# Kernel tuning notes

Measured on AMD Instinct MI355X. Metric: run time of the kernel, lower is better.

The kernel has to match this reference:

```python
import jax, jax.numpy as jnp
import numpy as np


def setup_inputs() -> dict:
    key = jax.random.key(0)
    k0, k1, k2, k3 = jax.random.split(key, 4)
    B, N, D, C, F = 8192, 784, 64, 10, 2  # batch, input_dim, bond_dim, num_classes, feature_dim
    x = jax.random.uniform(k0, (B, N), dtype=jnp.float32)  # pixel values in [0,1]
    core0 = jax.random.normal(k1, (F, 1, D), dtype=jnp.float32) * 0.1
    base = jnp.broadcast_to(jnp.eye(D, dtype=jnp.float32), (N - 2, F, D, D))
    cores_mid = base + jax.random.normal(k2, (N - 2, F, D, D), dtype=jnp.float32) * 0.01
    core_last = jax.random.normal(k3, (F, D, C), dtype=jnp.float32) * 0.1
    return {"x": x, "core0": core0, "cores_mid": cores_mid, "core_last": core_last}


def reference(x, core0, cores_mid, core_last):
    EPS = 1e-8
    factor = jnp.float32(np.pi / 2.0)
    # FeatureMap: [B, N] -> [B, N, 2] with (cos, sin)
    feats = jnp.stack([jnp.cos(factor * x), jnp.sin(factor * x)], axis=-1)
    # First site: M = v0 @ A0.squeeze(1)  -> [B, D]
    M = jnp.einsum('bf,fd->bd', feats[:, 0, :], core0[:, 0, :])
    # Sequential left->right contraction over middle sites with per-step L2 normalization
    v_mid = jnp.moveaxis(feats[:, 1:-1, :], 1, 0)  # [N-2, B, 2]

    def step(M, inp):
        v, A = inp  # v: [B, 2], A: [2, D, D]
        Mn = jnp.einsum('bi,bf,fij->bj', M, v, A)
        Mn = Mn / (jnp.linalg.norm(Mn, axis=1, keepdims=True) + EPS)
        return Mn, None

    M, _ = jax.lax.scan(step, M, (v_mid, cores_mid))
    # Last site: logits[b,c] = sum_i M[b,i] * (v_N[b,f] A_N[f,i,c])
    logits = jnp.einsum('bi,bf,fic->bc', M, feats[:, -1, :], core_last)
    return logits
```

## Files before the change

kernel.cpp:

```cpp
#include <hip/hip_runtime.h>

typedef __attribute__((ext_vector_type(8))) short s16x8;
typedef __attribute__((ext_vector_type(4))) float f32x4;
typedef __attribute__((ext_vector_type(4))) int i32x4;

#define NMID 782
#define PI_2 1.5707963267948966f
#define EG_STEP_BYTES 16384
#define EG_ELEMS ((size_t)NMID * 8192)
#define SLAB_B 2304

__device__ __forceinline__ int cvt_pk_bf16(float a, float b) {
  int r;
  asm("v_cvt_pk_bf16_f32 %0, %1, %2" : "=v"(r) : "v"(a), "v"(b));
  return r;
}

__device__ __forceinline__ f32x4 mfma_bf16(i32x4 a, i32x4 b, f32x4 c) {
  return __builtin_amdgcn_mfma_f32_16x16x32_bf16(
      __builtin_bit_cast(s16x8, a), __builtin_bit_cast(s16x8, b), c, 0, 0, 0);
}

__device__ __forceinline__ unsigned short bf16_rne(float v) {
  unsigned u = __float_as_uint(v);
  return (unsigned short)((u + 0x7FFFu + ((u >> 16) & 1)) >> 16);
}

__global__ __launch_bounds__(256) void prep_eg(const float* __restrict__ cm,
                                               unsigned short* __restrict__ eg) {
  const int n = blockIdx.x;
  const float* src = cm + (size_t)n * 8192;
  unsigned short* dst = eg + (size_t)n * 8192;
#pragma unroll
  for (int it = 0; it < 4; ++it) {
    int row = it * 256 + threadIdx.x;
    int q = row >> 6, l = row & 63;
    int t = q >> 2, cc = q & 3;
    int f = cc >> 1, c2 = cc & 1, h = l >> 4;
    int j = 16 * t + (l & 15);
    unsigned short v8[8];
#pragma unroll
    for (int e = 0; e < 8; ++e) {
      int i = 32 * c2 + 16 * (e >> 2) + 4 * h + (e & 3);
      float val = src[(f * 64 + i) * 64 + j] - (i == j ? 1.0f : 0.0f);
      v8[e] = bf16_rne(val);
    }
    *(uint4*)(dst + (size_t)row * 8) = *(const uint4*)v8;
  }
}

#define STEP4(nc, CUR, NXT, CC, SS)                                         \
  {                                                                         \
    int np = (nc) + 3;                                                      \
    if (np >= NMID) np = NMID - 1;                                          \
    const char* pnxt = base + (size_t)np * EG_STEP_BYTES;                   \
    _Pragma("unroll") for (int q = 0; q < 4; ++q)                           \
        NXT[q] = *(const i32x4*)(pnxt + q * 1024);                          \
    float cps = (CC) + (SS);                                                \
    f32x4 z = {0.f, 0.f, 0.f, 0.f};                                         \
    f32x4 accA = mfma_bf16(CUR[0], B0, z);                                  \
    accA = mfma_bf16(CUR[1], B1, accA);                                     \
    f32x4 accB = mfma_bf16(CUR[2], B0, z);                                  \
    accB = mfma_bf16(CUR[3], B1, accB);                                     \
    f32x4 mn;                                                               \
    _Pragma("unroll") for (int r = 0; r < 4; ++r)                           \
        mn[r] = cps * own4[r] + (CC)*accA[r] + (SS)*accB[r];                \
    own4 = mn;                                                              \
    int2 wq;                                                                \
    wq.x = cvt_pk_bf16(mn[0], mn[1]);                                       \
    wq.y = cvt_pk_bf16(mn[2], mn[3]);                                       \
    *(int2*)(xlds + (((nc) + 1) & 1) * SLAB_B + bl * 144 + h * 32 +         \
             wv * 8) = wq;                                                  \
    asm volatile("s_waitcnt lgkmcnt(0)" ::: "memory");                      \
    __builtin_amdgcn_s_barrier();                                           \
    __builtin_amdgcn_sched_barrier(0);                                      \
    {                                                                       \
      const char* rb =                                                      \
          xlds + (((nc) + 1) & 1) * SLAB_B + bl * 144 + h * 32;             \
      B0 = *(const i32x4*)(rb);                                             \
      B1 = *(const i32x4*)(rb + 16);                                        \
    }                                                                       \
  }

__global__ __launch_bounds__(256) void mps_main(
    const float* __restrict__ x, const float* __restrict__ core0,
    const float* __restrict__ core_last, const unsigned short* __restrict__ eg,
    float* __restrict__ out) {
  __shared__ alignas(16) char xlds[2 * SLAB_B];
  const int lane = threadIdx.x & 63;
  const int wv = threadIdx.x >> 6;
  const int bl = lane & 15;
  const int h = lane >> 4;
  const int b = blockIdx.x * 16 + bl;
  const float* xr = x + (size_t)b * 784;
  const char* base = (const char*)eg + (size_t)wv * 4096 + (size_t)lane * 16;

  f32x4 own4;
  i32x4 B0, B1;
  {
    float xv = xr[0];
    float s, c;
    __sincosf(PI_2 * xv, &s, &c);
    float fm[16];
#pragma unroll
    for (int t = 0; t < 4; ++t)
#pragma unroll
      for (int r = 0; r < 4; ++r) {
        int j = 16 * t + 4 * h + r;
        fm[t * 4 + r] = c * core0[j] + s * core0[64 + j];
      }
#pragma unroll
    for (int r = 0; r < 4; ++r) own4[r] = fm[wv * 4 + r];
#pragma unroll
    for (int p = 0; p < 4; ++p) {
      B0[p] = cvt_pk_bf16(fm[2 * p], fm[2 * p + 1]);
      B1[p] = cvt_pk_bf16(fm[8 + 2 * p], fm[8 + 2 * p + 1]);
    }
  }

  i32x4 frA[4], frB[4], frC[4], frD[4];
#pragma unroll
  for (int q = 0; q < 4; ++q)
    frA[q] = *(const i32x4*)(base + 0 * EG_STEP_BYTES + q * 1024);
#pragma unroll
  for (int q = 0; q < 4; ++q)
    frB[q] = *(const i32x4*)(base + 1 * EG_STEP_BYTES + q * 1024);
#pragma unroll
  for (int q = 0; q < 4; ++q)
    frC[q] = *(const i32x4*)(base + 2 * EG_STEP_BYTES + q * 1024);

  float xq[12], xqn[12];
  *(f32x4*)&xq[0] = *(const f32x4*)(xr + 0);
  *(f32x4*)&xq[4] = *(const f32x4*)(xr + 4);
  *(f32x4*)&xq[8] = *(const f32x4*)(xr + 8);

  for (int g = 0; g < 97; ++g) {
    if (g < 96) {
      const float* xp = xr + 8 * (g + 1);
      *(f32x4*)&xqn[0] = *(const f32x4*)(xp + 0);
      *(f32x4*)&xqn[4] = *(const f32x4*)(xp + 4);
      *(f32x4*)&xqn[8] = *(const f32x4*)(xp + 8);
    } else {
      *(f32x4*)&xqn[0] = *(const f32x4*)(xr + 776);
      *(f32x4*)&xqn[4] = *(const f32x4*)(xr + 780);
    }

    float cg[8], sg[8];
#pragma unroll
    for (int k = 0; k < 8; ++k) __sincosf(PI_2 * xq[1 + k], &sg[k], &cg[k]);

    if ((g & 7) == 0) {
      float ss = 0.f;
#pragma unroll
      for (int p = 0; p < 4; ++p) {
        unsigned u0 = (unsigned)B0[p], u1 = (unsigned)B1[p];
        float a0 = __uint_as_float(u0 << 16);
        float a1 = __uint_as_float(u0 & 0xFFFF0000u);
        float b0f = __uint_as_float(u1 << 16);
        float b1f = __uint_as_float(u1 & 0xFFFF0000u);
        ss += a0 * a0 + a1 * a1 + b0f * b0f + b1f * b1f;
      }
      ss += __shfl_xor(ss, 16);
      ss += __shfl_xor(ss, 32);
      float inv = rsqrtf(ss);
      cg[0] *= inv;
      sg[0] *= inv;
    }

    int n0 = 8 * g;
    STEP4(n0 + 0, frA, frD, cg[0], sg[0]);
    STEP4(n0 + 1, frB, frA, cg[1], sg[1]);
    STEP4(n0 + 2, frC, frB, cg[2], sg[2]);
    STEP4(n0 + 3, frD, frC, cg[3], sg[3]);
    STEP4(n0 + 4, frA, frD, cg[4], sg[4]);
    STEP4(n0 + 5, frB, frA, cg[5], sg[5]);
    STEP4(n0 + 6, frC, frB, cg[6], sg[6]);
    STEP4(n0 + 7, frD, frC, cg[7], sg[7]);

#pragma unroll
    for (int i = 0; i < 12; ++i) xq[i] = xqn[i];
  }

  {
    float cg[6], sg[6];
#pragma unroll
    for (int k = 0; k < 6; ++k) __sincosf(PI_2 * xq[1 + k], &sg[k], &cg[k]);
    STEP4(776, frA, frD, cg[0], sg[0]);
    STEP4(777, frB, frA, cg[1], sg[1]);
    STEP4(778, frC, frB, cg[2], sg[2]);
    STEP4(779, frD, frC, cg[3], sg[3]);
    STEP4(780, frA, frD, cg[4], sg[4]);
    STEP4(781, frB, frA, cg[5], sg[5]);
  }

  asm volatile("s_waitcnt lgkmcnt(0)" ::: "memory");
  __builtin_amdgcn_s_barrier();
  *(f32x4*)(xlds + wv * 1152 + lane * 16) = own4;
  asm volatile("s_waitcnt lgkmcnt(0)" ::: "memory");
  __builtin_amdgcn_s_barrier();
  __builtin_amdgcn_sched_barrier(0);
  float fm[16];
#pragma unroll
  for (int t = 0; t < 4; ++t) {
    f32x4 v = *(const f32x4*)(xlds + t * 1152 + lane * 16);
#pragma unroll
    for (int r = 0; r < 4; ++r) fm[t * 4 + r] = v[r];
  }

  float ss = 0.f;
#pragma unroll
  for (int i = 0; i < 16; ++i) ss += fm[i] * fm[i];
  ss += __shfl_xor(ss, 16);
  ss += __shfl_xor(ss, 32);
  float inv = 1.0f / (sqrtf(ss) + 1e-8f);
#pragma unroll
  for (int i = 0; i < 16; ++i) fm[i] *= inv;

  float xv = xq[7];
  float s, c;
  __sincosf(PI_2 * xv, &s, &c);
  float part[10];
#pragma unroll
  for (int cc = 0; cc < 10; ++cc) part[cc] = 0.f;
#pragma unroll
  for (int t = 0; t < 4; ++t)
#pragma unroll
    for (int r = 0; r < 4; ++r) {
      int i = 16 * t + 4 * h + r;
      float mv = fm[t * 4 + r];
#pragma unroll
      for (int cc = 0; cc < 10; ++cc)
        part[cc] += mv * (c * core_last[i * 10 + cc] + s * core_last[640 + i * 10 + cc]);
    }
#pragma unroll
  for (int cc = 0; cc < 10; ++cc) {
    part[cc] += __shfl_xor(part[cc], 16);
    part[cc] += __shfl_xor(part[cc], 32);
  }
  if (wv == 0 && h == 0) {
#pragma unroll
    for (int cc = 0; cc < 10; ++cc) out[b * 10 + cc] = part[cc];
  }
}

__global__ __launch_bounds__(64) void mps_slow(const float* __restrict__ x,
                                               const float* __restrict__ core0,
                                               const float* __restrict__ cm,
                                               const float* __restrict__ cl,
                                               float* __restrict__ out) {
  int b = blockIdx.x * 64 + threadIdx.x;
  float m[64], mn[64];
  float s, c;
  __sincosf(PI_2 * x[(size_t)b * 784], &s, &c);
  for (int d = 0; d < 64; ++d) m[d] = c * core0[d] + s * core0[64 + d];
  for (int n = 0; n < NMID; ++n) {
    __sincosf(PI_2 * x[(size_t)b * 784 + n + 1], &s, &c);
    const float* A0 = cm + (size_t)n * 8192;
    const float* A1 = A0 + 4096;
    for (int j = 0; j < 64; ++j) mn[j] = 0.f;
    for (int i = 0; i < 64; ++i) {
      float w0 = c * m[i], w1 = s * m[i];
      for (int j = 0; j < 64; ++j) mn[j] += w0 * A0[i * 64 + j] + w1 * A1[i * 64 + j];
    }
    float ssn = 0.f;
    for (int j = 0; j < 64; ++j) ssn += mn[j] * mn[j];
    float inv = 1.f / (sqrtf(ssn) + 1e-8f);
    for (int j = 0; j < 64; ++j) m[j] = mn[j] * inv;
  }
  __sincosf(PI_2 * x[(size_t)b * 784 + 783], &s, &c);
  for (int cc = 0; cc < 10; ++cc) {
    float acc = 0.f;
    for (int i = 0; i < 64; ++i)
      acc += m[i] * (c * cl[i * 10 + cc] + s * cl[640 + i * 10 + cc]);
    out[b * 10 + cc] = acc;
  }
}

extern "C" void kernel_launch(void* const* d_in, const int* in_sizes, int n_in,
                              void* d_out, int out_size, void* d_ws, size_t ws_size,
                              hipStream_t stream) {
  const float* x = (const float*)d_in[0];
  const float* core0 = (const float*)d_in[1];
  const float* cm = (const float*)d_in[2];
  const float* cl = (const float*)d_in[3];
  float* out = (float*)d_out;
  size_t need = EG_ELEMS * sizeof(unsigned short);
  if (ws_size >= need) {
    unsigned short* eg = (unsigned short*)d_ws;
    prep_eg<<<NMID, 256, 0, stream>>>(cm, eg);
    mps_main<<<512, 256, 0, stream>>>(x, core0, cl, eg, out);
  } else {
    mps_slow<<<8192 / 64, 64, 0, stream>>>(x, core0, cm, cl, out);
  }
}
```

Measured before the change: 267.9 us.

## Process two batch groups per block to reuse core fragments across MFMAs

```diff
diff --git a/kernel.cpp b/kernel.cpp
--- a/kernel.cpp
+++ b/kernel.cpp
@@ -9,6 +9,7 @@
 #define EG_STEP_BYTES 16384
 #define EG_ELEMS ((size_t)NMID * 8192)
 #define SLAB_B 2304
+#define DBUF_B 4608
 
 __device__ __forceinline__ int cvt_pk_bf16(float a, float b) {
   int r;
@@ -49,58 +50,77 @@
   }
 }
 
-#define STEP4(nc, CUR, NXT, CC, SS)                                         \
+#define STEP2G(nc, CUR, NXT, C0, S0, C1, S1)                                \
   {                                                                         \
     int np = (nc) + 3;                                                      \
     if (np >= NMID) np = NMID - 1;                                          \
     const char* pnxt = base + (size_t)np * EG_STEP_BYTES;                   \
     _Pragma("unroll") for (int q = 0; q < 4; ++q)                           \
         NXT[q] = *(const i32x4*)(pnxt + q * 1024);                          \
-    float cps = (CC) + (SS);                                                \
     f32x4 z = {0.f, 0.f, 0.f, 0.f};                                         \
-    f32x4 accA = mfma_bf16(CUR[0], B0, z);                                  \
-    accA = mfma_bf16(CUR[1], B1, accA);                                     \
-    f32x4 accB = mfma_bf16(CUR[2], B0, z);                                  \
-    accB = mfma_bf16(CUR[3], B1, accB);                                     \
-    f32x4 mn;                                                               \
+    __builtin_amdgcn_s_setprio(1);                                          \
+    f32x4 aA0 = mfma_bf16(CUR[0], B0g0, z);                                 \
+    aA0 = mfma_bf16(CUR[1], B1g0, aA0);                                     \
+    f32x4 aB0 = mfma_bf16(CUR[2], B0g0, z);                                 \
+    aB0 = mfma_bf16(CUR[3], B1g0, aB0);                                     \
+    f32x4 aA1 = mfma_bf16(CUR[0], B0g1, z);                                 \
+    aA1 = mfma_bf16(CUR[1], B1g1, aA1);                                     \
+    f32x4 aB1 = mfma_bf16(CUR[2], B0g1, z);                                 \
+    aB1 = mfma_bf16(CUR[3], B1g1, aB1);                                     \
+    __builtin_amdgcn_s_setprio(0);                                          \
+    char* wb = xlds + (((nc) + 1) & 1) * DBUF_B + bl * 144 + h * 32 +       \
+               wv * 8;                                                      \
+    float cps0 = (C0) + (S0);                                               \
+    f32x4 mn0;                                                              \
     _Pragma("unroll") for (int r = 0; r < 4; ++r)                           \
-        mn[r] = cps * own4[r] + (CC)*accA[r] + (SS)*accB[r];                \
-    own4 = mn;                                                              \
-    int2 wq;                                                                \
-    wq.x = cvt_pk_bf16(mn[0], mn[1]);                                       \
-    wq.y = cvt_pk_bf16(mn[2], mn[3]);                                       \
-    *(int2*)(xlds + (((nc) + 1) & 1) * SLAB_B + bl * 144 + h * 32 +         \
-             wv * 8) = wq;                                                  \
+        mn0[r] = cps0 * own0[r] + (C0)*aA0[r] + (S0)*aB0[r];                \
+    own0 = mn0;                                                             \
+    int2 w0;                                                                \
+    w0.x = cvt_pk_bf16(mn0[0], mn0[1]);                                     \
+    w0.y = cvt_pk_bf16(mn0[2], mn0[3]);                                     \
+    *(int2*)(wb) = w0;                                                      \
+    float cps1 = (C1) + (S1);                                               \
+    f32x4 mn1;                                                              \
+    _Pragma("unroll") for (int r = 0; r < 4; ++r)                           \
+        mn1[r] = cps1 * own1[r] + (C1)*aA1[r] + (S1)*aB1[r];                \
+    own1 = mn1;                                                             \
+    int2 w1;                                                                \
+    w1.x = cvt_pk_bf16(mn1[0], mn1[1]);                                     \
+    w1.y = cvt_pk_bf16(mn1[2], mn1[3]);                                     \
+    *(int2*)(wb + SLAB_B) = w1;                                             \
     asm volatile("s_waitcnt lgkmcnt(0)" ::: "memory");                      \
     __builtin_amdgcn_s_barrier();                                           \
     __builtin_amdgcn_sched_barrier(0);                                      \
     {                                                                       \
       const char* rb =                                                      \
-          xlds + (((nc) + 1) & 1) * SLAB_B + bl * 144 + h * 32;             \
-      B0 = *(const i32x4*)(rb);                                             \
-      B1 = *(const i32x4*)(rb + 16);                                        \
+          xlds + (((nc) + 1) & 1) * DBUF_B + bl * 144 + h * 32;             \
+      B0g0 = *(const i32x4*)(rb);                                           \
+      B1g0 = *(const i32x4*)(rb + 16);                                      \
+      B0g1 = *(const i32x4*)(rb + SLAB_B);                                  \
+      B1g1 = *(const i32x4*)(rb + SLAB_B + 16);                             \
     }                                                                       \
   }
 
-__global__ __launch_bounds__(256) void mps_main(
+__global__ __launch_bounds__(256, 1) void mps_main(
     const float* __restrict__ x, const float* __restrict__ core0,
     const float* __restrict__ core_last, const unsigned short* __restrict__ eg,
     float* __restrict__ out) {
-  __shared__ alignas(16) char xlds[2 * SLAB_B];
+  __shared__ alignas(16) char xlds[2 * DBUF_B];
   const int lane = threadIdx.x & 63;
   const int wv = threadIdx.x >> 6;
   const int bl = lane & 15;
   const int h = lane >> 4;
-  const int b = blockIdx.x * 16 + bl;
-  const float* xr = x + (size_t)b * 784;
+  const int b0 = blockIdx.x * 32 + bl;
+  const int b1 = b0 + 16;
+  const float* xr0 = x + (size_t)b0 * 784;
+  const float* xr1 = x + (size_t)b1 * 784;
   const char* base = (const char*)eg + (size_t)wv * 4096 + (size_t)lane * 16;
 
-  f32x4 own4;
-  i32x4 B0, B1;
+  f32x4 own0, own1;
+  i32x4 B0g0, B1g0, B0g1, B1g1;
   {
-    float xv = xr[0];
     float s, c;
-    __sincosf(PI_2 * xv, &s, &c);
+    __sincosf(PI_2 * xr0[0], &s, &c);
     float fm[16];
 #pragma unroll
     for (int t = 0; t < 4; ++t)
@@ -110,11 +130,30 @@
         fm[t * 4 + r] = c * core0[j] + s * core0[64 + j];
       }
 #pragma unroll
-    for (int r = 0; r < 4; ++r) own4[r] = fm[wv * 4 + r];
+    for (int r = 0; r < 4; ++r) own0[r] = fm[wv * 4 + r];
 #pragma unroll
     for (int p = 0; p < 4; ++p) {
-      B0[p] = cvt_pk_bf16(fm[2 * p], fm[2 * p + 1]);
-      B1[p] = cvt_pk_bf16(fm[8 + 2 * p], fm[8 + 2 * p + 1]);
+      B0g0[p] = cvt_pk_bf16(fm[2 * p], fm[2 * p + 1]);
+      B1g0[p] = cvt_pk_bf16(fm[8 + 2 * p], fm[8 + 2 * p + 1]);
+    }
+  }
+  {
+    float s, c;
+    __sincosf(PI_2 * xr1[0], &s, &c);
+    float fm[16];
+#pragma unroll
+    for (int t = 0; t < 4; ++t)
+#pragma unroll
+      for (int r = 0; r < 4; ++r) {
+        int j = 16 * t + 4 * h + r;
+        fm[t * 4 + r] = c * core0[j] + s * core0[64 + j];
+      }
+#pragma unroll
+    for (int r = 0; r < 4; ++r) own1[r] = fm[wv * 4 + r];
+#pragma unroll
+    for (int p = 0; p < 4; ++p) {
+      B0g1[p] = cvt_pk_bf16(fm[2 * p], fm[2 * p + 1]);
+      B1g1[p] = cvt_pk_bf16(fm[8 + 2 * p], fm[8 + 2 * p + 1]);
     }
   }
 
@@ -129,117 +168,153 @@
   for (int q = 0; q < 4; ++q)
     frC[q] = *(const i32x4*)(base + 2 * EG_STEP_BYTES + q * 1024);
 
-  float xq[12], xqn[12];
-  *(f32x4*)&xq[0] = *(const f32x4*)(xr + 0);
-  *(f32x4*)&xq[4] = *(const f32x4*)(xr + 4);
-  *(f32x4*)&xq[8] = *(const f32x4*)(xr + 8);
-
-  for (int g = 0; g < 97; ++g) {
-    if (g < 96) {
-      const float* xp = xr + 8 * (g + 1);
-      *(f32x4*)&xqn[0] = *(const f32x4*)(xp + 0);
-      *(f32x4*)&xqn[4] = *(const f32x4*)(xp + 4);
-      *(f32x4*)&xqn[8] = *(const f32x4*)(xp + 8);
+  float xq0[16], xqn0[16], xq1[16], xqn1[16];
+  *(f32x4*)&xq0[0] = *(const f32x4*)(xr0 + 0);
+  *(f32x4*)&xq0[4] = *(const f32x4*)(xr0 + 4);
+  *(f32x4*)&xq0[8] = *(const f32x4*)(xr0 + 8);
+  *(f32x4*)&xq0[12] = *(const f32x4*)(xr0 + 12);
+  *(f32x4*)&xq1[0] = *(const f32x4*)(xr1 + 0);
+  *(f32x4*)&xq1[4] = *(const f32x4*)(xr1 + 4);
+  *(f32x4*)&xq1[8] = *(const f32x4*)(xr1 + 8);
+  *(f32x4*)&xq1[12] = *(const f32x4*)(xr1 + 12);
+
+  for (int g = 0; g < 65; ++g) {
+    if (g < 64) {
+      const float* xp0 = xr0 + 12 * (g + 1);
+      *(f32x4*)&xqn0[0] = *(const f32x4*)(xp0 + 0);
+      *(f32x4*)&xqn0[4] = *(const f32x4*)(xp0 + 4);
+      *(f32x4*)&xqn0[8] = *(const f32x4*)(xp0 + 8);
+      *(f32x4*)&xqn0[12] = *(const f32x4*)(xp0 + 12);
+      const float* xp1 = xr1 + 12 * (g + 1);
+      *(f32x4*)&xqn1[0] = *(const f32x4*)(xp1 + 0);
+      *(f32x4*)&xqn1[4] = *(const f32x4*)(xp1 + 4);
+      *(f32x4*)&xqn1[8] = *(const f32x4*)(xp1 + 8);
+      *(f32x4*)&xqn1[12] = *(const f32x4*)(xp1 + 12);
     } else {
-      *(f32x4*)&xqn[0] = *(const f32x4*)(xr + 776);
-      *(f32x4*)&xqn[4] = *(const f32x4*)(xr + 780);
-    }
-
-    float cg[8], sg[8];
-#pragma unroll
-    for (int k = 0; k < 8; ++k) __sincosf(PI_2 * xq[1 + k], &sg[k], &cg[k]);
-
-    if ((g & 7) == 0) {
-      float ss = 0.f;
+      *(f32x4*)&xqn0[0] = *(const f32x4*)(xr0 + 780);
+      *(f32x4*)&xqn1[0] = *(const f32x4*)(xr1 + 780);
+    }
+
+    float cg0[12], sg0[12], cg1[12], sg1[12];
+#pragma unroll
+    for (int k = 0; k < 12; ++k) {
+      __sincosf(PI_2 * xq0[1 + k], &sg0[k], &cg0[k]);
+      __sincosf(PI_2 * xq1[1 + k], &sg1[k], &cg1[k]);
+    }
+
+    if (g % 5 == 0) {
+      float ss0 = 0.f, ss1 = 0.f;
 #pragma unroll
       for (int p = 0; p < 4; ++p) {
-        unsigned u0 = (unsigned)B0[p], u1 = (unsigned)B1[p];
+        unsigned u0 = (unsigned)B0g0[p], u1 = (unsigned)B1g0[p];
         float a0 = __uint_as_float(u0 << 16);
         float a1 = __uint_as_float(u0 & 0xFFFF0000u);
-        float b0f = __uint_as_float(u1 << 16);
-        float b1f = __uint_as_float(u1 & 0xFFFF0000u);
-        ss += a0 * a0 + a1 * a1 + b0f * b0f + b1f * b1f;
+        float d0 = __uint_as_float(u1 << 16);
+        float d1 = __uint_as_float(u1 & 0xFFFF0000u);
+        ss0 += a0 * a0 + a1 * a1 + d0 * d0 + d1 * d1;
+        unsigned v0 = (unsigned)B0g1[p], v1 = (unsigned)B1g1[p];
+        float e0 = __uint_as_float(v0 << 16);
+        float e1 = __uint_as_float(v0 & 0xFFFF0000u);
+        float f0 = __uint_as_float(v1 << 16);
+        float f1 = __uint_as_float(v1 & 0xFFFF0000u);
+        ss1 += e0 * e0 + e1 * e1 + f0 * f0 + f1 * f1;
       }
-      ss += __shfl_xor(ss, 16);
-      ss += __shfl_xor(ss, 32);
-      float inv = rsqrtf(ss);
-      cg[0] *= inv;
-      sg[0] *= inv;
-    }
-
-    int n0 = 8 * g;
-    STEP4(n0 + 0, frA, frD, cg[0], sg[0]);
-    STEP4(n0 + 1, frB, frA, cg[1], sg[1]);
-    STEP4(n0 + 2, frC, frB, cg[2], sg[2]);
-    STEP4(n0 + 3, frD, frC, cg[3], sg[3]);
-    STEP4(n0 + 4, frA, frD, cg[4], sg[4]);
-    STEP4(n0 + 5, frB, frA, cg[5], sg[5]);
-    STEP4(n0 + 6, frC, frB, cg[6], sg[6]);
-    STEP4(n0 + 7, frD, frC, cg[7], sg[7]);
-
-#pragma unroll
-    for (int i = 0; i < 12; ++i) xq[i] = xqn[i];
+      ss0 += __shfl_xor(ss0, 16);
+      ss0 += __shfl_xor(ss0, 32);
+      ss1 += __shfl_xor(ss1, 16);
+      ss1 += __shfl_xor(ss1, 32);
+      float inv0 = rsqrtf(ss0), inv1 = rsqrtf(ss1);
+      cg0[0] *= inv0;
+      sg0[0] *= inv0;
+      cg1[0] *= inv1;
+      sg1[0] *= inv1;
+    }
+
+    int n0 = 12 * g;
+    STEP2G(n0 + 0, frA, frD, cg0[0], sg0[0], cg1[0], sg1[0]);
+    STEP2G(n0 + 1, frB, frA, cg0[1], sg0[1], cg1[1], sg1[1]);
+    STEP2G(n0 + 2, frC, frB, cg0[2], sg0[2], cg1[2], sg1[2]);
+    STEP2G(n0 + 3, frD, frC, cg0[3], sg0[3], cg1[3], sg1[3]);
+    STEP2G(n0 + 4, frA, frD, cg0[4], sg0[4], cg1[4], sg1[4]);
+    STEP2G(n0 + 5, frB, frA, cg0[5], sg0[5], cg1[5], sg1[5]);
+    STEP2G(n0 + 6, frC, frB, cg0[6], sg0[6], cg1[6], sg1[6]);
+    STEP2G(n0 + 7, frD, frC, cg0[7], sg0[7], cg1[7], sg1[7]);
+    STEP2G(n0 + 8, frA, frD, cg0[8], sg0[8], cg1[8], sg1[8]);
+    STEP2G(n0 + 9, frB, frA, cg0[9], sg0[9], cg1[9], sg1[9]);
+    STEP2G(n0 + 10, frC, frB, cg0[10], sg0[10], cg1[10], sg1[10]);
+    STEP2G(n0 + 11, frD, frC, cg0[11], sg0[11], cg1[11], sg1[11]);
+
+#pragma unroll
+    for (int i = 0; i < 16; ++i) {
+      xq0[i] = xqn0[i];
+      xq1[i] = xqn1[i];
+    }
   }
 
   {
-    float cg[6], sg[6];
-#pragma unroll
-    for (int k = 0; k < 6; ++k) __sincosf(PI_2 * xq[1 + k], &sg[k], &cg[k]);
-    STEP4(776, frA, frD, cg[0], sg[0]);
-    STEP4(777, frB, frA, cg[1], sg[1]);
-    STEP4(778, frC, frB, cg[2], sg[2]);
-    STEP4(779, frD, frC, cg[3], sg[3]);
-    STEP4(780, frA, frD, cg[4], sg[4]);
-    STEP4(781, frB, frA, cg[5], sg[5]);
+    float c00, s00, c01, s01, c10, s10, c11, s11;
+    __sincosf(PI_2 * xq0[1], &s00, &c00);
+    __sincosf(PI_2 * xq0[2], &s01, &c01);
+    __sincosf(PI_2 * xq1[1], &s10, &c10);
+    __sincosf(PI_2 * xq1[2], &s11, &c11);
+    STEP2G(780, frA, frD, c00, s00, c10, s10);
+    STEP2G(781, frB, frA, c01, s01, c11, s11);
   }
 
   asm volatile("s_waitcnt lgkmcnt(0)" ::: "memory");
   __builtin_amdgcn_s_barrier();
-  *(f32x4*)(xlds + wv * 1152 + lane * 16) = own4;
+  *(f32x4*)(xlds + wv * 1152 + lane * 16) = own0;
+  *(f32x4*)(xlds + DBUF_B + wv * 1152 + lane * 16) = own1;
   asm volatile("s_waitcnt lgkmcnt(0)" ::: "memory");
   __builtin_amdgcn_s_barrier();
   __builtin_amdgcn_sched_barrier(0);
-  float fm[16];
-#pragma unroll
-  for (int t = 0; t < 4; ++t) {
-    f32x4 v = *(const f32x4*)(xlds + t * 1152 + lane * 16);
-#pragma unroll
-    for (int r = 0; r < 4; ++r) fm[t * 4 + r] = v[r];
-  }
-
-  float ss = 0.f;
-#pragma unroll
-  for (int i = 0; i < 16; ++i) ss += fm[i] * fm[i];
-  ss += __shfl_xor(ss, 16);
-  ss += __shfl_xor(ss, 32);
-  float inv = 1.0f / (sqrtf(ss) + 1e-8f);
-#pragma unroll
-  for (int i = 0; i < 16; ++i) fm[i] *= inv;
-
-  float xv = xq[7];
-  float s, c;
-  __sincosf(PI_2 * xv, &s, &c);
-  float part[10];
-#pragma unroll
-  for (int cc = 0; cc < 10; ++cc) part[cc] = 0.f;
-#pragma unroll
-  for (int t = 0; t < 4; ++t)
-#pragma unroll
-    for (int r = 0; r < 4; ++r) {
-      int i = 16 * t + 4 * h + r;
-      float mv = fm[t * 4 + r];
-#pragma unroll
-      for (int cc = 0; cc < 10; ++cc)
-        part[cc] += mv * (c * core_last[i * 10 + cc] + s * core_last[640 + i * 10 + cc]);
-    }
-#pragma unroll
-  for (int cc = 0; cc < 10; ++cc) {
-    part[cc] += __shfl_xor(part[cc], 16);
-    part[cc] += __shfl_xor(part[cc], 32);
-  }
-  if (wv == 0 && h == 0) {
-#pragma unroll
-    for (int cc = 0; cc < 10; ++cc) out[b * 10 + cc] = part[cc];
+
+#pragma unroll
+  for (int grp = 0; grp < 2; ++grp) {
+    float fm[16];
+#pragma unroll
+    for (int t = 0; t < 4; ++t) {
+      f32x4 v =
+          *(const f32x4*)(xlds + grp * DBUF_B + t * 1152 + lane * 16);
+#pragma unroll
+      for (int r = 0; r < 4; ++r) fm[t * 4 + r] = v[r];
+    }
+    float ss = 0.f;
+#pragma unroll
+    for (int i = 0; i < 16; ++i) ss += fm[i] * fm[i];
+    ss += __shfl_xor(ss, 16);
+    ss += __shfl_xor(ss, 32);
+    float inv = 1.0f / (sqrtf(ss) + 1e-8f);
+#pragma unroll
+    for (int i = 0; i < 16; ++i) fm[i] *= inv;
+
+    float xv = grp == 0 ? xq0[3] : xq1[3];
+    float s, c;
+    __sincosf(PI_2 * xv, &s, &c);
+    float part[10];
+#pragma unroll
+    for (int cc = 0; cc < 10; ++cc) part[cc] = 0.f;
+#pragma unroll
+    for (int t = 0; t < 4; ++t)
+#pragma unroll
+      for (int r = 0; r < 4; ++r) {
+        int i = 16 * t + 4 * h + r;
+        float mv = fm[t * 4 + r];
+#pragma unroll
+        for (int cc = 0; cc < 10; ++cc)
+          part[cc] +=
+              mv * (c * core_last[i * 10 + cc] + s * core_last[640 + i * 10 + cc]);
+      }
+#pragma unroll
+    for (int cc = 0; cc < 10; ++cc) {
+      part[cc] += __shfl_xor(part[cc], 16);
+      part[cc] += __shfl_xor(part[cc], 32);
+    }
+    if (wv == 0 && h == 0) {
+      int brow = grp == 0 ? b0 : b1;
+#pragma unroll
+      for (int cc = 0; cc < 10; ++cc) out[brow * 10 + cc] = part[cc];
+    }
   }
 }
 
@@ -288,7 +363,7 @@
   if (ws_size >= need) {
     unsigned short* eg = (unsigned short*)d_ws;
     prep_eg<<<NMID, 256, 0, stream>>>(cm, eg);
-    mps_main<<<512, 256, 0, stream>>>(x, core0, cl, eg, out);
+    mps_main<<<256, 256, 0, stream>>>(x, core0, cl, eg, out);
   } else {
     mps_slow<<<8192 / 64, 64, 0, stream>>>(x, core0, cm, cl, out);
   }
```

New measurement: 279.4 us. 1.04x slower.
